# Kernel optimization log

Hardware: AMD Instinct MI355X
Metric: run time of the kernel (lower is better)

The kernel has to match this reference:

```python
import jax, jax.numpy as jnp
import numpy as np

B, S, D, H, W = 2, 8192, 512, 8, 256   # batch, seq, d_model, heads, one-sided window
HD = D // H                            # head dim = 64
C = S // W                             # number of chunks of size W (seq % 2W == 0 holds)


def setup_inputs() -> dict:
    key = jax.random.key(0)
    ks = jax.random.split(key, 7)
    x = jax.random.normal(ks[0], (B, S, D), jnp.float32)
    def w(k):
        return jax.random.normal(k, (D, D), jnp.float32) * 0.02
    def b(k):
        return jax.random.normal(k, (D,), jnp.float32) * 0.02
    return {
        "x": x,
        "Wq": w(ks[1]), "bq": b(ks[2]),
        "Wk": w(ks[3]), "bk": b(ks[4]),
        "Wv": w(ks[5]), "bv": b(ks[6]),
    }


def _heads_chunked(t):
    # (B,S,D) -> (B*H, C, W, HD): split heads, then split sequence into chunks of W
    return t.reshape(B, S, H, HD).transpose(0, 2, 1, 3).reshape(B * H, C, W, HD)


def _three_chunks(t):
    # neighbor-chunk concat: for chunk c, gather chunks [c-1, c, c+1] (zero padded at ends)
    tp = jnp.pad(t, ((0, 0), (1, 1), (0, 0), (0, 0)))
    return jnp.concatenate([tp[:, :-2], tp[:, 1:-1], tp[:, 2:]], axis=2)  # (B*H, C, 3W, HD)


def reference(x, Wq, bq, Wk, bk, Wv, bv):
    scale = 1.0 / np.sqrt(HD)
    q = _heads_chunked((x @ Wq + bq) * scale)
    k = _heads_chunked(x @ Wk + bk)
    v = _heads_chunked(x @ Wv + bv)

    k3 = _three_chunks(k)
    v3 = _three_chunks(v)

    # chunk-local scores against 3 neighboring chunks: (B*H, C, W, 3W)
    scores = jnp.einsum('bcxd,bcyd->bcxy', q, k3)

    # extract the (2W+1)-wide diagonal band: query x attends keys x..x+2W in the 3W window
    rows = jnp.arange(W)[:, None]                       # (W,1)
    diag = rows + jnp.arange(2 * W + 1)[None, :]        # (W, 2W+1) indices into 3W axis
    band = jnp.take_along_axis(scores, diag[None, None], axis=3)  # (B*H, C, W, 2W+1)

    # mask band entries whose global key position falls outside [0, S)
    pos = jnp.arange(S).reshape(C, W)[:, :, None] + (jnp.arange(2 * W + 1) - W)  # (C,W,2W+1)
    valid = (pos >= 0) & (pos < S)
    band = jnp.where(valid[None], band, -jnp.inf)

    probs = jax.nn.softmax(band, axis=-1)  # (B*H, C, W, 2W+1)

    # scatter band probs back into (W, 3W) layout and contract with values
    full = jnp.zeros((B * H, C, W, 3 * W), probs.dtype).at[:, :, rows, diag].set(probs)
    out = jnp.einsum('bcxy,bcyd->bcxd', full, v3)  # (B*H, C, W, HD)

    return out.reshape(B, H, S, HD).transpose(0, 2, 1, 3).reshape(B, S, D)
```

## Files before the change

kernel.cpp:

```cpp
#include <hip/hip_runtime.h>
#include <hip/hip_bf16.h>

#define S_LEN 8192
#define D_MODEL 512
#define NH 8
#define HD 64
#define WIN 256
#define NB 2

#define QSCALE 0.1803368801111204f

#define EXP2N(x) __builtin_amdgcn_exp2f(x)

typedef __hip_bfloat16 bf16;
typedef __attribute__((ext_vector_type(8))) short short8;
typedef __attribute__((ext_vector_type(4))) float f32x4;

static __device__ __forceinline__ short f2bf(float f) {
    bf16 h = __float2bfloat16(f);
    return *reinterpret_cast<short*>(&h);
}

static __device__ __forceinline__ void gload_lds16(short* lds, const short* g) {
    __builtin_amdgcn_global_load_lds(
        (const __attribute__((address_space(1))) void*)g,
        (__attribute__((address_space(3))) void*)lds, 16, 0, 0);
}

__global__ __launch_bounds__(256) void convert_x_kernel(
    const float* __restrict__ x, short* __restrict__ xb)
{
    const int n4 = (NB * S_LEN * D_MODEL) / 4;
    for (int i = blockIdx.x * 256 + threadIdx.x; i < n4; i += gridDim.x * 256) {
        float4 v = ((const float4*)x)[i];
        short4 o;
        o.x = f2bf(v.x); o.y = f2bf(v.y); o.z = f2bf(v.z); o.w = f2bf(v.w);
        ((short4*)xb)[i] = o;
    }
}

__global__ __launch_bounds__(256) void convert_wT_kernel(
    const float* __restrict__ Wq, const float* __restrict__ Wk,
    const float* __restrict__ Wv, short* __restrict__ wT)
{
    __shared__ float t[32][33];
    const float* W = blockIdx.z == 0 ? Wq : (blockIdx.z == 1 ? Wk : Wv);
    const int n0 = blockIdx.x * 32, k0 = blockIdx.y * 32;
    const int tx = threadIdx.x & 31, ty = threadIdx.x >> 5;
#pragma unroll
    for (int i = 0; i < 4; ++i)
        t[ty + 8 * i][tx] = W[(size_t)(k0 + ty + 8 * i) * D_MODEL + n0 + tx];
    __syncthreads();
#pragma unroll
    for (int i = 0; i < 4; ++i) {
        const int nl = ty + 8 * i, kl = tx;
        wT[(size_t)blockIdx.z * D_MODEL * D_MODEL +
           (size_t)(n0 + nl) * D_MODEL + k0 + kl] = f2bf(t[kl][nl]);
    }
}

__global__ __launch_bounds__(256) void proj_mfma_kernel(
    const short* __restrict__ xb, const short* __restrict__ wT,
    const float* __restrict__ bq, const float* __restrict__ bk,
    const float* __restrict__ bv, bf16* __restrict__ qkv)
{
    __shared__ short Ash[128 * 64];
    __shared__ short Bsh[128 * 64];

    const int nwg  = gridDim.x * gridDim.y;
    const int orig = blockIdx.y * gridDim.x + blockIdx.x;
    const int wid  = (orig & 7) * (nwg >> 3) + (orig >> 3);
    const int bx   = wid % 12;
    const int by   = wid / 12;

    const int widx = bx >> 2;
    const int col0 = (bx & 3) * 128;
    const int row0 = by * 128;
    const int tid  = threadIdx.x;
    const int w    = tid >> 6;
    const int lane = tid & 63;
    const int col  = lane & 15;
    const int kg   = lane >> 4;

    const float* bias = widx == 0 ? bq : (widx == 1 ? bk : bv);
    const float scale = widx == 0 ? QSCALE : 1.0f;
    const short* wbase = wT + (size_t)widx * D_MODEL * D_MODEL;

    const f32x4 zero4 = {0.f, 0.f, 0.f, 0.f};
    f32x4 acc[4][4];
#pragma unroll
    for (int i = 0; i < 4; ++i)
#pragma unroll
        for (int j = 0; j < 4; ++j) acc[i][j] = zero4;

    const int wm0 = (w >> 1) * 64;
    const int wn0 = (w & 1) * 64;

    for (int kb = 0; kb < D_MODEL; kb += 64) {
#pragma unroll
        for (int ci = 0; ci < 4; ++ci) {
            const int Lb = w * 256 + ci * 64;
            const int L  = Lb + lane;
            const int m  = L >> 3;
            const int kc = ((L & 7) - (m >> 1)) & 7;
            const int ko = kb + kc * 8;
            gload_lds16(Ash + (size_t)Lb * 8,
                        xb + (size_t)(row0 + m) * D_MODEL + ko);
            gload_lds16(Bsh + (size_t)Lb * 8,
                        wbase + (size_t)(col0 + m) * D_MODEL + ko);
        }
        __syncthreads();

#pragma unroll
        for (int s = 0; s < 2; ++s) {
            short8 af[4], bfr[4];
#pragma unroll
            for (int mt = 0; mt < 4; ++mt) {
                const int m = wm0 + mt * 16 + col;
                const int c = m * 8 + ((s * 4 + kg + (m >> 1)) & 7);
                af[mt] = *(const short8*)(Ash + (size_t)c * 8);
            }
#pragma unroll
            for (int nt = 0; nt < 4; ++nt) {
                const int n = wn0 + nt * 16 + col;
                const int c = n * 8 + ((s * 4 + kg + (n >> 1)) & 7);
                bfr[nt] = *(const short8*)(Bsh + (size_t)c * 8);
            }
#pragma unroll
            for (int mt = 0; mt < 4; ++mt)
#pragma unroll
                for (int nt = 0; nt < 4; ++nt)
                    acc[mt][nt] = __builtin_amdgcn_mfma_f32_16x16x32_bf16(
                        af[mt], bfr[nt], acc[mt][nt], 0, 0, 0);
        }
        __syncthreads();
    }

    bf16* dst = qkv + (size_t)widx * (NB * NH * S_LEN * HD);
#pragma unroll
    for (int nt = 0; nt < 4; ++nt) {
        const int n = col0 + wn0 + nt * 16 + col;
        const float bias_v = bias[n];
        const int h = n >> 6, d = n & 63;
#pragma unroll
        for (int mt = 0; mt < 4; ++mt) {
            const int m0 = row0 + wm0 + mt * 16 + kg * 4;
            const int b = m0 >> 13, s0 = m0 & (S_LEN - 1);
            if (widx == 2) {
                short4 pk;
                pk.x = f2bf(acc[mt][nt][0] + bias_v);
                pk.y = f2bf(acc[mt][nt][1] + bias_v);
                pk.z = f2bf(acc[mt][nt][2] + bias_v);
                pk.w = f2bf(acc[mt][nt][3] + bias_v);
                *(short4*)&dst[(((size_t)(b * NH + h)) * HD + d) * S_LEN + s0] = pk;
            } else {
#pragma unroll
                for (int r = 0; r < 4; ++r)
                    dst[(((size_t)(b * NH + h)) * S_LEN + s0 + r) * HD + d] =
                        __float2bfloat16((acc[mt][nt][r] + bias_v) * scale);
            }
        }
    }
}

__global__ __launch_bounds__(256) void proj_kernel(
    const float* __restrict__ x, const float* __restrict__ Wm,
    const float* __restrict__ bias, bf16* __restrict__ dst, float scale,
    int transpose_v)
{
    __shared__ float As[16][64];
    __shared__ float Bs[16][64];
    const int tid  = threadIdx.x;
    const int row0 = blockIdx.y * 64;
    const int col0 = blockIdx.x * 64;
    const int ty = tid >> 4, tx = tid & 15;
    const int t4 = tid * 4;
    const int ai = t4 >> 4, aj = t4 & 15;
    const int bj = t4 >> 6, bi = t4 & 63;
    float acc[4][4] = {};
    for (int kb = 0; kb < D_MODEL; kb += 16) {
        float4 av = *(const float4*)(x  + (size_t)(row0 + ai) * D_MODEL + kb + aj);
        float4 bv = *(const float4*)(Wm + (size_t)(kb + bj)  * D_MODEL + col0 + bi);
        As[aj + 0][ai] = av.x; As[aj + 1][ai] = av.y;
        As[aj + 2][ai] = av.z; As[aj + 3][ai] = av.w;
        *(float4*)(&Bs[bj][bi]) = bv;
        __syncthreads();
#pragma unroll
        for (int k = 0; k < 16; ++k) {
            float a[4], b[4];
#pragma unroll
            for (int ii = 0; ii < 4; ++ii) a[ii] = As[k][ty * 4 + ii];
#pragma unroll
            for (int jj = 0; jj < 4; ++jj) b[jj] = Bs[k][tx * 4 + jj];
#pragma unroll
            for (int ii = 0; ii < 4; ++ii)
#pragma unroll
                for (int jj = 0; jj < 4; ++jj) acc[ii][jj] += a[ii] * b[jj];
        }
        __syncthreads();
    }
#pragma unroll
    for (int ii = 0; ii < 4; ++ii) {
        const int m = row0 + ty * 4 + ii;
        const int b = m >> 13, s = m & (S_LEN - 1);
#pragma unroll
        for (int jj = 0; jj < 4; ++jj) {
            const int n = col0 + tx * 4 + jj;
            const int h = n >> 6, d = n & 63;
            const float v = (acc[ii][jj] + bias[n]) * scale;
            if (transpose_v)
                dst[(((size_t)(b * NH + h)) * HD + d) * S_LEN + s] = __float2bfloat16(v);
            else
                dst[(((size_t)(b * NH + h)) * S_LEN + s) * HD + d] = __float2bfloat16(v);
        }
    }
}

__global__ __launch_bounds__(512) void attn_mfma5_kernel(
    const bf16* __restrict__ qw, const bf16* __restrict__ kw,
    const bf16* __restrict__ vt, float* __restrict__ out)
{
    __shared__ __align__(16) short Ksh[2][4096];
    __shared__ __align__(16) short Vsh[2][4096];
    __shared__ __align__(16) short Psh[8][16][72];

    const int orig = blockIdx.y * gridDim.x + blockIdx.x;
    const int wf   = (orig & 7) * 128 + (orig >> 3);
    const int bh   = wf >> 6;
    const int qt0  = (wf & 63) * 128;

    const int tid  = threadIdx.x;
    const int w    = tid >> 6;
    const int lane = tid & 63;
    const int col  = lane & 15;
    const int kg   = lane >> 4;
    const int q0   = qt0 + w * 16;
    const int q    = q0 + col;
    const size_t base = (size_t)bh * S_LEN * HD;

    const short* qg  = (const short*)qw;
    const short* kgp = (const short*)kw;
    const short* vgp = (const short*)vt;

    const int kt_lo = qt0 - WIN < 0 ? 0 : qt0 - WIN;
    const int kt_hi0 = qt0 + WIN + 64;
    const int kt_hi = kt_hi0 > S_LEN - 64 ? S_LEN - 64 : kt_hi0;
    const int NT    = ((kt_hi - kt_lo) >> 6) + 1;

    const int r0 = tid >> 3, c0 = (tid & 7) ^ (r0 & 7);
    const int ldsb = w * 64 * 8;

    const short* qptr = qg + base + (size_t)q * HD + kg * 8;
    const short8 qB0 = *(const short8*)(qptr);
    const short8 qB1 = *(const short8*)(qptr + 32);

    const f32x4 zero4 = {0.f, 0.f, 0.f, 0.f};
    f32x4 Oacc[4] = {zero4, zero4, zero4, zero4};
    float m = -1e30f, l = 0.f;

    const int x7 = col & 7;

    gload_lds16(&Ksh[0][ldsb], kgp + base + (size_t)(kt_lo + r0) * HD + c0 * 8);
    gload_lds16(&Vsh[0][ldsb], vgp + base + (size_t)r0 * S_LEN + kt_lo + c0 * 8);

    for (int i = 0; i < NT; ++i) {
        __syncthreads();

        if (i + 1 < NT) {
            const int ktn = kt_lo + 64 * (i + 1);
            const int nb = (i + 1) & 1;
            gload_lds16(&Ksh[nb][ldsb], kgp + base + (size_t)(ktn + r0) * HD + c0 * 8);
            gload_lds16(&Vsh[nb][ldsb], vgp + base + (size_t)r0 * S_LEN + ktn + c0 * 8);
        }

        const int kt = kt_lo + 64 * i;
        const short* Kb = Ksh[i & 1];
        const short* Vb = Vsh[i & 1];

        f32x4 sc[4];
        __builtin_amdgcn_s_setprio(1);
#pragma unroll
        for (int t = 0; t < 4; ++t) {
            const int key = 16 * t + col;
            const short8 kA0 = *(const short8*)(Kb + (size_t)(key * 8 + (kg ^ x7)) * 8);
            const short8 kA1 = *(const short8*)(Kb + (size_t)(key * 8 + ((kg + 4) ^ x7)) * 8);
            f32x4 a = zero4;
            a = __builtin_amdgcn_mfma_f32_16x16x32_bf16(kA0, qB0, a, 0, 0, 0);
            a = __builtin_amdgcn_mfma_f32_16x16x32_bf16(kA1, qB1, a, 0, 0, 0);
            sc[t] = a;
        }
        __builtin_amdgcn_s_setprio(0);

        const bool need_mask = (kt < q0 + 15 - WIN) || (kt + 63 > q0 + WIN);
        if (need_mask) {
#pragma unroll
            for (int t = 0; t < 4; ++t)
#pragma unroll
                for (int r = 0; r < 4; ++r) {
                    const int j = kt + 16 * t + kg * 4 + r;
                    if (j < q - WIN || j > q + WIN) sc[t][r] = -1e30f;
                }
        }

        float tm0 = fmaxf(fmaxf(sc[0][0], sc[0][1]), fmaxf(sc[0][2], sc[0][3]));
        float tm1 = fmaxf(fmaxf(sc[1][0], sc[1][1]), fmaxf(sc[1][2], sc[1][3]));
        float tm2 = fmaxf(fmaxf(sc[2][0], sc[2][1]), fmaxf(sc[2][2], sc[2][3]));
        float tm3 = fmaxf(fmaxf(sc[3][0], sc[3][1]), fmaxf(sc[3][2], sc[3][3]));
        float tmax = fmaxf(fmaxf(tm0, tm1), fmaxf(tm2, tm3));
        tmax = fmaxf(tmax, __shfl_xor(tmax, 16));
        tmax = fmaxf(tmax, __shfl_xor(tmax, 32));

        if (__any(tmax > m + 8.f)) {
            const float mnew = fmaxf(m, tmax);
            const float alpha = EXP2N(m - mnew);
            m = mnew;
#pragma unroll
            for (int dt = 0; dt < 4; ++dt)
#pragma unroll
                for (int r = 0; r < 4; ++r) Oacc[dt][r] *= alpha;
            l *= alpha;
        }

        float p[4][4];
#pragma unroll
        for (int t = 0; t < 4; ++t)
#pragma unroll
            for (int r = 0; r < 4; ++r) p[t][r] = EXP2N(sc[t][r] - m);

        float r0s = (p[0][0] + p[0][1]) + (p[0][2] + p[0][3]);
        float r1s = (p[1][0] + p[1][1]) + (p[1][2] + p[1][3]);
        float r2s = (p[2][0] + p[2][1]) + (p[2][2] + p[2][3]);
        float r3s = (p[3][0] + p[3][1]) + (p[3][2] + p[3][3]);
        float rs = (r0s + r1s) + (r2s + r3s);
        rs += __shfl_xor(rs, 16);
        rs += __shfl_xor(rs, 32);
        l += rs;

#pragma unroll
        for (int t = 0; t < 4; ++t) {
            short4 pk;
            pk.x = f2bf(p[t][0]); pk.y = f2bf(p[t][1]);
            pk.z = f2bf(p[t][2]); pk.w = f2bf(p[t][3]);
            *(short4*)&Psh[w][col][16 * t + 4 * kg] = pk;
        }

        const short* pp = &Psh[w][col][kg * 8];
        const short8 pB0 = *(const short8*)(pp);
        const short8 pB1 = *(const short8*)(pp + 32);

        __builtin_amdgcn_s_setprio(1);
#pragma unroll
        for (int dt = 0; dt < 4; ++dt) {
            const int d = dt * 16 + col;
            const short8 vA0 = *(const short8*)(Vb + (size_t)(d * 8 + (kg ^ x7)) * 8);
            const short8 vA1 = *(const short8*)(Vb + (size_t)(d * 8 + ((kg + 4) ^ x7)) * 8);
            Oacc[dt] = __builtin_amdgcn_mfma_f32_16x16x32_bf16(vA0, pB0, Oacc[dt], 0, 0, 0);
            Oacc[dt] = __builtin_amdgcn_mfma_f32_16x16x32_bf16(vA1, pB1, Oacc[dt], 0, 0, 0);
        }
        __builtin_amdgcn_s_setprio(0);
    }

    const float inv = 1.0f / l;
    const int b = bh >> 3, h = bh & 7;
    float* op = out + ((size_t)(b * S_LEN + q)) * D_MODEL + h * HD + kg * 4;
#pragma unroll
    for (int dt = 0; dt < 4; ++dt) {
        float4 o;
        o.x = Oacc[dt][0] * inv; o.y = Oacc[dt][1] * inv;
        o.z = Oacc[dt][2] * inv; o.w = Oacc[dt][3] * inv;
        *(float4*)(op + dt * 16) = o;
    }
}

extern "C" void kernel_launch(void* const* d_in, const int* in_sizes, int n_in,
                              void* d_out, int out_size, void* d_ws, size_t ws_size,
                              hipStream_t stream)
{
    const float* x  = (const float*)d_in[0];
    const float* Wq = (const float*)d_in[1];
    const float* bq = (const float*)d_in[2];
    const float* Wk = (const float*)d_in[3];
    const float* bk = (const float*)d_in[4];
    const float* Wv = (const float*)d_in[5];
    const float* bv = (const float*)d_in[6];
    float* out = (float*)d_out;

    const size_t n_elem = (size_t)NB * NH * S_LEN * HD;
    bf16* qw = (bf16*)d_ws;
    bf16* kw = qw + n_elem;
    bf16* vw = kw + n_elem;
    short* xb = (short*)(vw + n_elem);
    short* wT = xb + (size_t)NB * S_LEN * D_MODEL;

    const size_t need = (3 * n_elem + (size_t)NB * S_LEN * D_MODEL +
                         3 * (size_t)D_MODEL * D_MODEL) * sizeof(short);

    if (ws_size >= need) {
        convert_x_kernel<<<2048, 256, 0, stream>>>(x, xb);
        dim3 wgrid(D_MODEL / 32, D_MODEL / 32, 3);
        convert_wT_kernel<<<wgrid, 256, 0, stream>>>(Wq, Wk, Wv, wT);
        dim3 ggrid(12, (NB * S_LEN) / 128);
        proj_mfma_kernel<<<ggrid, 256, 0, stream>>>(xb, wT, bq, bk, bv, qw);
    } else {
        dim3 pgrid(D_MODEL / 64, (NB * S_LEN) / 64);
        proj_kernel<<<pgrid, 256, 0, stream>>>(x, Wq, bq, qw, QSCALE, 0);
        proj_kernel<<<pgrid, 256, 0, stream>>>(x, Wk, bk, kw, 1.0f, 0);
        proj_kernel<<<pgrid, 256, 0, stream>>>(x, Wv, bv, vw, 1.0f, 1);
    }

    dim3 agrid(NB * NH, S_LEN / 128);
    attn_mfma5_kernel<<<agrid, 512, 0, stream>>>(qw, kw, vw, out);
}
```

Measured before the change: 177.5 us.

## Feed P to PV MFMA from registers using 16x16x16 bf16 instructions

Replaces the LDS round-trip for the softmax probabilities with a register path. The exp results already sit in the layout that the B operand of mfma_f32_16x16x16bf16_1k expects, so each 16-key slice is packed and fed straight into the PV MMA. This removes the Psh write and read and any need to order them. In exchange it issues twice as many MFMAs, each half as wide as the 16x16x32 form, and V loads become 4-element reads. It also adds launch-bound occupancy hints and pads Vsh.

```diff
diff --git a/kernel.cpp b/kernel.cpp
--- a/kernel.cpp
+++ b/kernel.cpp
@@ -12,8 +12,15 @@
 
 #define EXP2N(x) __builtin_amdgcn_exp2f(x)
 
+#if __has_builtin(__builtin_amdgcn_mfma_f32_16x16x16bf16_1k)
+#define PV_REG_PATH 1
+#else
+#define PV_REG_PATH 0
+#endif
+
 typedef __hip_bfloat16 bf16;
 typedef __attribute__((ext_vector_type(8))) short short8;
+typedef __attribute__((ext_vector_type(4))) short bf16x4;
 typedef __attribute__((ext_vector_type(4))) float f32x4;
 
 static __device__ __forceinline__ short f2bf(float f) {
@@ -216,13 +223,15 @@
     }
 }
 
-__global__ __launch_bounds__(512) void attn_mfma5_kernel(
+__global__ __launch_bounds__(512, 8) void attn_mfma5_kernel(
     const bf16* __restrict__ qw, const bf16* __restrict__ kw,
     const bf16* __restrict__ vt, float* __restrict__ out)
 {
     __shared__ __align__(16) short Ksh[2][4096];
-    __shared__ __align__(16) short Vsh[2][4096];
+    __shared__ __align__(16) short Vsh[2][4096 + 128];
+#if !PV_REG_PATH
     __shared__ __align__(16) short Psh[8][16][72];
+#endif
 
     const int orig = blockIdx.y * gridDim.x + blockIdx.x;
     const int wf   = (orig & 7) * 128 + (orig >> 3);
@@ -321,33 +330,48 @@
             l *= alpha;
         }
 
-        float p[4][4];
 #pragma unroll
         for (int t = 0; t < 4; ++t)
 #pragma unroll
-            for (int r = 0; r < 4; ++r) p[t][r] = EXP2N(sc[t][r] - m);
-
-        float r0s = (p[0][0] + p[0][1]) + (p[0][2] + p[0][3]);
-        float r1s = (p[1][0] + p[1][1]) + (p[1][2] + p[1][3]);
-        float r2s = (p[2][0] + p[2][1]) + (p[2][2] + p[2][3]);
-        float r3s = (p[3][0] + p[3][1]) + (p[3][2] + p[3][3]);
+            for (int r = 0; r < 4; ++r) sc[t][r] = EXP2N(sc[t][r] - m);
+
+        float r0s = (sc[0][0] + sc[0][1]) + (sc[0][2] + sc[0][3]);
+        float r1s = (sc[1][0] + sc[1][1]) + (sc[1][2] + sc[1][3]);
+        float r2s = (sc[2][0] + sc[2][1]) + (sc[2][2] + sc[2][3]);
+        float r3s = (sc[3][0] + sc[3][1]) + (sc[3][2] + sc[3][3]);
         float rs = (r0s + r1s) + (r2s + r3s);
         rs += __shfl_xor(rs, 16);
         rs += __shfl_xor(rs, 32);
         l += rs;
 
+#if PV_REG_PATH
+        __builtin_amdgcn_s_setprio(1);
+#pragma unroll
+        for (int t = 0; t < 4; ++t) {
+            bf16x4 pBt;
+            pBt[0] = f2bf(sc[t][0]); pBt[1] = f2bf(sc[t][1]);
+            pBt[2] = f2bf(sc[t][2]); pBt[3] = f2bf(sc[t][3]);
+            const int cot = (((2 * t + (kg >> 1)) ^ x7) << 3) + ((kg & 1) << 2);
+#pragma unroll
+            for (int dt = 0; dt < 4; ++dt) {
+                const int d = dt * 16 + col;
+                const bf16x4 vA = *(const bf16x4*)(Vb + (size_t)d * 64 + cot);
+                Oacc[dt] = __builtin_amdgcn_mfma_f32_16x16x16bf16_1k(
+                    vA, pBt, Oacc[dt], 0, 0, 0);
+            }
+        }
+        __builtin_amdgcn_s_setprio(0);
+#else
 #pragma unroll
         for (int t = 0; t < 4; ++t) {
             short4 pk;
-            pk.x = f2bf(p[t][0]); pk.y = f2bf(p[t][1]);
-            pk.z = f2bf(p[t][2]); pk.w = f2bf(p[t][3]);
+            pk.x = f2bf(sc[t][0]); pk.y = f2bf(sc[t][1]);
+            pk.z = f2bf(sc[t][2]); pk.w = f2bf(sc[t][3]);
             *(short4*)&Psh[w][col][16 * t + 4 * kg] = pk;
         }
-
         const short* pp = &Psh[w][col][kg * 8];
         const short8 pB0 = *(const short8*)(pp);
         const short8 pB1 = *(const short8*)(pp + 32);
-
         __builtin_amdgcn_s_setprio(1);
 #pragma unroll
         for (int dt = 0; dt < 4; ++dt) {
@@ -358,6 +382,7 @@
             Oacc[dt] = __builtin_amdgcn_mfma_f32_16x16x32_bf16(vA1, pB1, Oacc[dt], 0, 0, 0);
         }
         __builtin_amdgcn_s_setprio(0);
+#endif
     }
 
     const float inv = 1.0f / l;
```

After: 227.9 us. 28.4% more time.
